# Kernel optimization log

Hardware: AMD Instinct MI355X
Metric: run time of the kernel (lower is better)

## Reference

```python
import jax, jax.numpy as jnp
import numpy as np

TAU_MEM = 20.0
TAU_SYN = 5.0
THRESHOLD = 1.0
SURROGATE_BETA = 4.0
RESET_POTENTIAL = 0.0

B, T, D_IN, H = 32, 1024, 512, 512


def setup_inputs() -> dict:
    key = jax.random.key(0)
    k1, k2 = jax.random.split(key)
    inputs = jax.random.normal(k1, (B, T, D_IN), dtype=jnp.float32)
    kernel = jax.random.normal(k2, (D_IN, H), dtype=jnp.float32) / np.sqrt(D_IN)
    bias = jnp.zeros((H,), dtype=jnp.float32)
    return {"inputs": inputs, "kernel": kernel, "bias": bias}


def reference(inputs, kernel, bias):
    batch = inputs.shape[0]
    hidden = kernel.shape[1]
    alpha_mem = jnp.exp(jnp.float32(-1.0 / TAU_MEM))
    alpha_syn = jnp.exp(jnp.float32(-1.0 / TAU_SYN))

    # Batch the per-step dense GEMM across time: [B,T,Din] @ [Din,H] -> [B,T,H]
    currents = jnp.einsum('bti,ih->bth', inputs, kernel) + bias
    currents_t = jnp.swapaxes(currents, 0, 1)  # [T,B,H] for scan

    def step(carry, ic):
        v_mem, i_syn = carry
        i_syn = alpha_syn * i_syn + ic
        v_mem = alpha_mem * v_mem + (1.0 - alpha_mem) * i_syn
        spikes = (v_mem >= THRESHOLD).astype(jnp.float32)
        surrogate = SURROGATE_BETA / (2.0 * (1.0 + jnp.cosh(SURROGATE_BETA * (v_mem - THRESHOLD))))
        spikes_with_grad = spikes + jax.lax.stop_gradient(spikes - surrogate)
        v_mem = jnp.where(spikes > 0, RESET_POTENTIAL, v_mem)
        return (v_mem, i_syn), (spikes_with_grad, v_mem)

    init = (jnp.zeros((batch, hidden), jnp.float32), jnp.zeros((batch, hidden), jnp.float32))
    (v_final, _), (spikes_t, vmem_t) = jax.lax.scan(step, init, currents_t)

    spike_output = jnp.swapaxes(spikes_t, 0, 1)      # [B,T,H]
    membrane_states = jnp.swapaxes(vmem_t, 0, 1)     # [B,T,H]
    spike_rate = jnp.mean(spike_output)
    return spike_output, membrane_states, v_final, spike_rate
```

## Files before the change

kernel.cpp:

```cpp
#include <hip/hip_runtime.h>

typedef unsigned short ushort_t;
typedef unsigned int   uint_t;
typedef float    float4v __attribute__((ext_vector_type(4)));
typedef _Float16 h16x8   __attribute__((ext_vector_type(8)));

#define Bsz 32
#define Tsz 1024
#define Din 512
#define Hsz 512
#define Mtot (Bsz * Tsz)
#define ELEMS ((size_t)Mtot * Hsz)

#define GLL16(gp, lp) __builtin_amdgcn_global_load_lds(                        \
    (const __attribute__((address_space(1))) unsigned int*)(gp),               \
    (__attribute__((address_space(3))) unsigned int*)(lp), 16, 0, 0)

#define GLL4(gp, lp) __builtin_amdgcn_global_load_lds(                         \
    (const __attribute__((address_space(1))) unsigned int*)(gp),               \
    (__attribute__((address_space(3))) unsigned int*)(lp), 4, 0, 0)

__global__ __launch_bounds__(256) void split_fp16x2(
    const float* __restrict__ A, const float* __restrict__ W,
    _Float16* __restrict__ Ah, _Float16* __restrict__ Bh)
{
    const int bid = blockIdx.x, tid = threadIdx.x;
    if (bid < 4096) {
        const size_t e   = ((size_t)bid * 256 + tid) * 16;
        const int    row = (int)(e >> 9);
        const int    col = (int)(e & 511);
        const float4* Af = (const float4*)(A + e);
        h16x8 v0a, v1a, v0b, v1b;
#pragma unroll
        for (int q = 0; q < 4; ++q) {
            float4 x = Af[q];
            const float c[4] = {x.x, x.y, x.z, x.w};
#pragma unroll
            for (int j = 0; j < 4; ++j) {
                const float xs = c[j] * 256.0f;
                const _Float16 h0 = (_Float16)xs;
                const float rf = xs - (float)h0;
                const _Float16 h1 = (_Float16)rf;
                const int idx = q * 4 + j;
                if (idx < 8) { v0a[idx] = h0; v1a[idx] = h1; }
                else         { v0b[idx - 8] = h0; v1b[idx - 8] = h1; }
            }
        }
        _Float16* d0 = Ah + (size_t)row * 1024 + col;
        *(h16x8*)(d0)           = v0a;
        *(h16x8*)(d0 + 8)       = v0b;
        *(h16x8*)(d0 + 512)     = v1a;
        *(h16x8*)(d0 + 512 + 8) = v1b;
    } else {
        const int f4 = (bid - 4096) * 256 + tid;
        const int k  = f4 >> 7;
        const int n4 = (f4 & 127) << 2;
        float4 x = *(const float4*)(W + (size_t)k * Hsz + n4);
        const float c[4] = {x.x, x.y, x.z, x.w};
#pragma unroll
        for (int j = 0; j < 4; ++j) {
            const float ws = c[j] * 2048.0f;
            const _Float16 h0 = (_Float16)ws;
            const float rf = ws - (float)h0;
            const _Float16 h1 = (_Float16)rf;
            _Float16* d = Bh + (size_t)(n4 + j) * 1024 + k;
            d[0]   = h0;
            d[512] = h1;
        }
    }
}

#define SA_STAGE(LIMB, KK, SLOTBASE) do {                                      \
    const char* g_ = Ag + (size_t)((LIMB) * 1024) + (size_t)((KK) * 64);       \
    _Pragma("unroll") for (int H = 0; H < 4; ++H)                              \
        GLL16(g_ + (size_t)H * 131072, ldsA + (SLOTBASE) + H * 4096 + lsd);    \
} while (0)

#define SB_STAGE(LIMB, KK, SLOT) do {                                          \
    const char* g_ = Bg + (size_t)((LIMB) * 1024) + (size_t)((KK) * 64);       \
    _Pragma("unroll") for (int H = 0; H < 2; ++H)                              \
        GLL16(g_ + (size_t)H * 131072, ldsB + (SLOT) * 8192 + H * 4096 + lsd); \
} while (0)

#define LD_AF(SLOTBASE) do {                                                   \
    _Pragma("unroll") for (int mf = 0; mf < 8; ++mf)                           \
        af[mf] = *(const h16x8*)(ldsA + (SLOTBASE) + (wm + mf * 16 + lr) * 64  \
                                 + physf * 16);                                \
} while (0)

#define LD_BF(DST, SLOT) do {                                                  \
    _Pragma("unroll") for (int nf = 0; nf < 4; ++nf)                           \
        DST[nf] = *(const h16x8*)(ldsB + (SLOT) * 8192 + (wn + nf * 16 + lr)   \
                                  * 64 + physf * 16);                          \
} while (0)

#define MFMAH(BF) do { __builtin_amdgcn_s_setprio(1);                          \
    _Pragma("unroll") for (int mf = 0; mf < 8; ++mf)                           \
    _Pragma("unroll") for (int nf = 0; nf < 4; ++nf)                           \
        acc[mf][nf] = __builtin_amdgcn_mfma_f32_16x16x32_f16(                  \
            af[mf], BF[nf], acc[mf][nf], 0, 0, 0);                             \
    __builtin_amdgcn_s_setprio(0); } while (0)

#define GATE(N) do { asm volatile("s_waitcnt vmcnt(" #N ")" ::: "memory");     \
    __builtin_amdgcn_sched_barrier(0); __builtin_amdgcn_s_barrier();           \
    asm volatile("" ::: "memory"); } while (0)

__global__ __launch_bounds__(256, 2) void gemm_f16k3(
    const _Float16* __restrict__ Ah, const _Float16* __restrict__ Bh,
    const float* __restrict__ bias, float* __restrict__ C)
{
    __shared__ __align__(16) char lds[65536];
    char* ldsA = lds;
    char* ldsB = lds + 32768;

    const int tid = threadIdx.x;
    const int bid = blockIdx.x;
    const int lin = ((bid & 7) << 6) | (bid >> 3);
    const int m0  = (lin >> 2) << 8;
    const int n0  = (lin & 3) << 7;
    const int w = tid >> 6, lane = tid & 63;
    const int wm = (w & 1) << 7;
    const int wn = (w >> 1) << 6;
    const int lr = lane & 15, lg = lane >> 4;

    const int physf = lg ^ (lr & 3) ^ ((lr >> 2) & 3);

    const int srow = tid >> 2;
    const int schk = tid & 3;
    const int logchk = schk ^ (srow & 3) ^ ((srow >> 2) & 3);
    const int lsd = tid * 16;
    const char* Ag = (const char*)Ah + (size_t)(m0 + srow) * 2048 + logchk * 16;
    const char* Bg = (const char*)Bh + (size_t)(n0 + srow) * 2048 + logchk * 16;

    float4v acc[8][4];
#pragma unroll
    for (int i = 0; i < 8; ++i)
#pragma unroll
        for (int j = 0; j < 4; ++j) acc[i][j] = (float4v)0.f;

    h16x8 af[8], bf0[4], bf1[4];

    SA_STAGE(0, 0, 0);
    SB_STAGE(0, 0, 0); SB_STAGE(1, 0, 1);
    SB_STAGE(0, 1, 2); SB_STAGE(1, 1, 3);
    GATE(0);

#pragma unroll 1
    for (int k = 0; k < 15; ++k) {
        const int s0 = (2 * k) & 3, s1 = (2 * k + 1) & 3;
        GATE(4);
        LD_AF(0); LD_BF(bf0, s0);
        SA_STAGE(1, k, 16384);
        MFMAH(bf0);
        GATE(4);
        LD_BF(bf1, s1);
        SA_STAGE(0, k + 1, 0);
        MFMAH(bf1);
        GATE(4);
        LD_AF(16384);
        if (k < 14) { SB_STAGE(0, k + 2, s0); SB_STAGE(1, k + 2, s1); }
        MFMAH(bf0);
    }
    {
        GATE(0);
        LD_AF(0); LD_BF(bf0, 2);
        SA_STAGE(1, 15, 16384);
        MFMAH(bf0);
        GATE(4);
        LD_BF(bf1, 3);
        MFMAH(bf1);
        GATE(0);
        LD_AF(16384);
        MFMAH(bf0);
    }

    constexpr float INVS = 1.0f / 524288.0f;
#pragma unroll
    for (int nf = 0; nf < 4; ++nf) {
        const int col = n0 + wn + nf * 16 + lr;
        const float bv = bias[col];
#pragma unroll
        for (int mf = 0; mf < 8; ++mf)
#pragma unroll
            for (int j = 0; j < 4; ++j) {
                const int row = m0 + wm + mf * 16 + lg * 4 + j;
                C[(size_t)row * Hsz + col] = fmaf(acc[mf][nf][j], INVS, bv);
            }
    }
}

#define BM 128
#define BN 128
#define BK 16
#define LDSA (BM + 4)
#define LDSB (BN + 4)
__global__ __launch_bounds__(256) void sgemm_currents(
    const float* __restrict__ A, const float* __restrict__ B,
    const float* __restrict__ bias, float* __restrict__ C)
{
    __shared__ float As[BK][LDSA];
    __shared__ float Bs[BK][LDSB];
    const int tid = threadIdx.x;
    const int tx = tid & 15, ty = tid >> 4;
    const int m0 = blockIdx.y * BM, n0 = blockIdx.x * BN;
    const int arow = tid >> 2, ac4 = (tid & 3) * 4;
    const int brow = tid >> 5, bc4 = (tid & 31) * 4;
    float acc[8][8];
#pragma unroll
    for (int i = 0; i < 8; ++i)
#pragma unroll
        for (int j = 0; j < 8; ++j) acc[i][j] = 0.f;
    const float* Abase = A + (size_t)(m0 + arow) * Din + ac4;
    const float* Bbase = B + (size_t)brow * Hsz + n0 + bc4;
    float4 a0 = *(const float4*)Abase;
    float4 a1 = *(const float4*)(Abase + (size_t)64 * Din);
    float4 b0 = *(const float4*)Bbase;
    float4 b1 = *(const float4*)(Bbase + (size_t)8 * Hsz);
    const int NKT = Din / BK;
    for (int kt = 0; kt < NKT; ++kt) {
        const float* apf = (const float*)&a0;
        const float* aqf = (const float*)&a1;
#pragma unroll
        for (int j = 0; j < 4; ++j) As[ac4 + j][arow] = apf[j];
#pragma unroll
        for (int j = 0; j < 4; ++j) As[ac4 + j][arow + 64] = aqf[j];
        *(float4*)&Bs[brow][bc4] = b0;
        *(float4*)&Bs[brow + 8][bc4] = b1;
        __syncthreads();
        if (kt + 1 < NKT) {
            const float* An = Abase + (kt + 1) * BK;
            const float* Bn = Bbase + (size_t)(kt + 1) * BK * Hsz;
            a0 = *(const float4*)An;
            a1 = *(const float4*)(An + (size_t)64 * Din);
            b0 = *(const float4*)Bn;
            b1 = *(const float4*)(Bn + (size_t)8 * Hsz);
        }
#pragma unroll
        for (int k = 0; k < BK; ++k) {
            float4 af0 = *(const float4*)&As[k][ty * 8];
            float4 af1 = *(const float4*)&As[k][ty * 8 + 4];
            float4 bf0 = *(const float4*)&Bs[k][tx * 8];
            float4 bf1 = *(const float4*)&Bs[k][tx * 8 + 4];
            const float av[8] = {af0.x, af0.y, af0.z, af0.w, af1.x, af1.y, af1.z, af1.w};
            const float bv[8] = {bf0.x, bf0.y, bf0.z, bf0.w, bf1.x, bf1.y, bf1.z, bf1.w};
#pragma unroll
            for (int i = 0; i < 8; ++i)
#pragma unroll
                for (int j = 0; j < 8; ++j) acc[i][j] = fmaf(av[i], bv[j], acc[i][j]);
        }
        __syncthreads();
    }
    const float4 bi0 = *(const float4*)&bias[n0 + tx * 8];
    const float4 bi1 = *(const float4*)&bias[n0 + tx * 8 + 4];
#pragma unroll
    for (int i = 0; i < 8; ++i) {
        const size_t row = (size_t)(m0 + ty * 8 + i);
        float4 o0 = make_float4(acc[i][0] + bi0.x, acc[i][1] + bi0.y,
                                acc[i][2] + bi0.z, acc[i][3] + bi0.w);
        float4 o1 = make_float4(acc[i][4] + bi1.x, acc[i][5] + bi1.y,
                                acc[i][6] + bi1.z, acc[i][7] + bi1.w);
        float* cp = C + row * Hsz + n0 + tx * 8;
        *(float4*)cp = o0;
        *(float4*)(cp + 4) = o1;
    }
}

__global__ __launch_bounds__(64) void lif_scan_g(
    const float* __restrict__ cur, float* __restrict__ spikes,
    float* __restrict__ vmem, float* __restrict__ vfinal,
    float* __restrict__ partials)
{
    __shared__ __align__(16) float lbuf[2][32][64];

    constexpr float A_M  = 0.95122942450071400910f;
    constexpr float OM_M = 1.0f - A_M;
    constexpr float A_S  = 0.81873075307798182354f;

    const int tid   = threadIdx.x;
    const int bid   = blockIdx.x;
    const int batch = bid >> 3;
    const int hbase = (bid & 7) << 6;
    const size_t sbase = (size_t)batch * (size_t)(Tsz * Hsz) + hbase + tid;

    const float* gsrc = cur + sbase;
    float* gspk = spikes + sbase;
    float* gvmm = vmem + sbase;

#pragma unroll
    for (int r = 0; r < 32; ++r)
        GLL4(gsrc + r * 512, &lbuf[0][r][0]);
    asm volatile("s_waitcnt vmcnt(0)" ::: "memory");
    __builtin_amdgcn_sched_barrier(0);

    float v = 0.f, isyn = 0.f, acc = 0.f;
    int pb = 0;
#pragma unroll 1
    for (int c = 0; c < 32; ++c) {
        if (c < 31) {
            const float* gs = gsrc + (size_t)(c + 1) * 16384;
            float (*db)[64] = lbuf[pb ^ 1];
#pragma unroll
            for (int r = 0; r < 32; ++r)
                GLL4(gs + r * 512, &db[r][0]);
        }
        const float* lrow = &lbuf[pb][0][tid];
        float* sp = gspk + (size_t)c * 16384;
        float* vp = gvmm + (size_t)c * 16384;
#pragma unroll
        for (int r = 0; r < 32; ++r) {
            isyn = fmaf(A_S, isyn, lrow[r * 64]);
            v    = fmaf(A_M, v, OM_M * isyn);
            const bool sb = (v >= 1.0f);
            float x = fminf(fmaf(4.0f, v, -4.0f), 30.0f);
            const float ep = __expf(x);
            const float tt = 1.0f + ep;
            const float rr = __builtin_amdgcn_rcpf(tt * tt);
            const float s2 = sb ? 2.0f : 0.0f;
            const float so = fmaf(-4.0f * ep, rr, s2);
            v = sb ? 0.0f : v;
            acc += so;
            sp[r * 512] = so;
            vp[r * 512] = v;
        }
        asm volatile("s_waitcnt vmcnt(63)" ::: "memory");
        __builtin_amdgcn_sched_barrier(0);
        pb ^= 1;
    }

    vfinal[bid * 64 + tid] = v;
#pragma unroll
    for (int o = 32; o; o >>= 1) acc += __shfl_down(acc, o);
    if (tid == 0) partials[blockIdx.x] = acc;
}

__device__ __forceinline__ void lif_step(float c, float& v, float& isyn,
                                         float& so_out)
{
    constexpr float A_M  = 0.95122942450071400910f;
    constexpr float OM_M = 1.0f - A_M;
    constexpr float A_S  = 0.81873075307798182354f;
    isyn = fmaf(A_S, isyn, c);
    v    = fmaf(A_M, v, OM_M * isyn);
    const float sp = (v >= 1.0f) ? 1.0f : 0.0f;
    float x = fmaf(4.0f, v, -4.0f);
    x = fminf(x, 30.0f);
    const float ep = __expf(x);
    const float tt = 1.0f + ep;
    const float surr = 4.0f * ep * __builtin_amdgcn_rcpf(tt * tt);
    so_out = fmaf(2.0f, sp, -surr);
    v = (sp > 0.f) ? 0.0f : v;
}

__global__ __launch_bounds__(64) void lif_scan(
    const float* cur, float* spikes, float* vmem, float* vfinal, float* partials)
{
    const int tid = threadIdx.x;
    const int gid = blockIdx.x * 64 + tid;
    const size_t base = ((size_t)(gid >> 9)) * (size_t)Tsz * Hsz + (gid & 511);

    float v = 0.f, isyn = 0.f, acc = 0.f;
    constexpr int P = 8;
    float ring[P];
#pragma unroll
    for (int p = 0; p < P; ++p) ring[p] = cur[base + (size_t)p * Hsz];

    for (int t = 0; t < Tsz; t += P) {
#pragma unroll
        for (int p = 0; p < P; ++p) {
            const float c = ring[p];
            int tn = t + P + p;
            tn = tn < (Tsz - 1) ? tn : (Tsz - 1);
            ring[p] = cur[base + (size_t)tn * Hsz];

            float so;
            lif_step(c, v, isyn, so);
            const size_t idx = base + (size_t)(t + p) * Hsz;
            spikes[idx] = so;
            vmem[idx]   = v;
            acc += so;
        }
    }
    vfinal[gid] = v;
#pragma unroll
    for (int off = 32; off; off >>= 1) acc += __shfl_down(acc, off);
    if (tid == 0) partials[blockIdx.x] = acc;
}

__global__ __launch_bounds__(256) void rate_finalize(
    const float* __restrict__ partials, float* __restrict__ rate)
{
    const int tid = threadIdx.x;
    float s = partials[tid];
#pragma unroll
    for (int off = 32; off; off >>= 1) s += __shfl_down(s, off);
    __shared__ float wsum[4];
    if ((tid & 63) == 0) wsum[tid >> 6] = s;
    __syncthreads();
    if (tid == 0)
        rate[0] = ((wsum[0] + wsum[1]) + (wsum[2] + wsum[3])) * (1.0f / 16777216.0f);
}

extern "C" void kernel_launch(void* const* d_in, const int* in_sizes, int n_in,
                              void* d_out, int out_size, void* d_ws, size_t ws_size,
                              hipStream_t stream)
{
    const float* inputs = (const float*)d_in[0];
    const float* weight = (const float*)d_in[1];
    const float* bias   = (const float*)d_in[2];

    float* out    = (float*)d_out;
    float* spikes = out;
    float* vmem   = out + ELEMS;
    float* vfinal = out + 2 * ELEMS;
    float* rate   = vfinal + (size_t)Bsz * Hsz;

    float* partials = (float*)d_ws;
    char*  ws       = (char*)d_ws;

    const size_t HDR   = 16384;
    const size_t CUR_B = ELEMS * 4;
    const size_t AH_B  = (size_t)Mtot * 1024 * 2;
    const size_t BH_B  = (size_t)Hsz * 1024 * 2;

    _Float16 *Ah, *Bh;
    float* cur;
    int path;
    if (ws_size >= HDR + CUR_B + AH_B + BH_B) {
        cur = (float*)(ws + HDR);
        Ah  = (_Float16*)(ws + HDR + CUR_B);
        Bh  = Ah + (size_t)Mtot * 1024;
        path = 0;
    } else if (ws_size >= HDR + CUR_B) {
        cur = (float*)(ws + HDR);
        Ah  = (_Float16*)d_out;
        Bh  = Ah + (size_t)Mtot * 1024;
        path = 1;
    } else {
        cur = vmem;
        Ah = Bh = nullptr;
        path = 2;
    }

    if (path != 2) {
        split_fp16x2<<<dim3(4096 + 256), 256, 0, stream>>>(inputs, weight, Ah, Bh);
        gemm_f16k3<<<dim3(512), 256, 0, stream>>>(Ah, Bh, bias, cur);
        lif_scan_g<<<dim3(256), 64, 0, stream>>>(cur, spikes, vmem, vfinal, partials);
    } else {
        sgemm_currents<<<dim3(4, 256), 256, 0, stream>>>(inputs, weight, bias, cur);
        lif_scan<<<dim3(256), 64, 0, stream>>>(cur, spikes, vmem, vfinal, partials);
    }
    rate_finalize<<<dim3(1), 256, 0, stream>>>(partials, rate);
}
```

Before: 150.0 us.

## Split LIF scan into producer and consumer wavefronts via LDS

The LIF scan kernel now runs two wavefronts per block. One loads currents and runs only the serial recurrence, writing pre-reset membrane values to a double-buffered LDS array. The other reads those values, computes spikes and surrogate outputs, and does the global stores and the rate reduction. The aim is to take the exp/rcp work and store traffic off the serial critical path so it overlaps with the recurrence. The cost is extra LDS, a block barrier per chunk, and a producer that waits on both vmcnt and lgkmcnt each chunk.

```diff
diff --git a/kernel.cpp b/kernel.cpp
--- a/kernel.cpp
+++ b/kernel.cpp
@@ -265,72 +265,95 @@
     }
 }
 
-__global__ __launch_bounds__(64) void lif_scan_g(
+__global__ __launch_bounds__(128) void lif_scan_pc(
     const float* __restrict__ cur, float* __restrict__ spikes,
     float* __restrict__ vmem, float* __restrict__ vfinal,
     float* __restrict__ partials)
 {
     __shared__ __align__(16) float lbuf[2][32][64];
+    __shared__ __align__(16) float pbuf[2][32][64];
 
     constexpr float A_M  = 0.95122942450071400910f;
     constexpr float OM_M = 1.0f - A_M;
     constexpr float A_S  = 0.81873075307798182354f;
 
-    const int tid   = threadIdx.x;
-    const int bid   = blockIdx.x;
+    const int tid  = threadIdx.x;
+    const int lane = tid & 63;
+    const int wv   = tid >> 6;
+    const int bid  = blockIdx.x;
     const int batch = bid >> 3;
     const int hbase = (bid & 7) << 6;
-    const size_t sbase = (size_t)batch * (size_t)(Tsz * Hsz) + hbase + tid;
-
-    const float* gsrc = cur + sbase;
-    float* gspk = spikes + sbase;
-    float* gvmm = vmem + sbase;
-
-#pragma unroll
-    for (int r = 0; r < 32; ++r)
-        GLL4(gsrc + r * 512, &lbuf[0][r][0]);
-    asm volatile("s_waitcnt vmcnt(0)" ::: "memory");
-    __builtin_amdgcn_sched_barrier(0);
-
-    float v = 0.f, isyn = 0.f, acc = 0.f;
-    int pb = 0;
+    const size_t sbase = (size_t)batch * (size_t)(Tsz * Hsz) + hbase + lane;
+
+    if (wv == 0) {
+        const float* gsrc = cur + sbase;
+#pragma unroll
+        for (int r = 0; r < 32; ++r)
+            GLL4(gsrc + r * 512, &lbuf[0][r][0]);
+        asm volatile("s_waitcnt vmcnt(0)" ::: "memory");
+        __builtin_amdgcn_sched_barrier(0);
+
+        float v = 0.f, isyn = 0.f;
 #pragma unroll 1
-    for (int c = 0; c < 32; ++c) {
-        if (c < 31) {
-            const float* gs = gsrc + (size_t)(c + 1) * 16384;
-            float (*db)[64] = lbuf[pb ^ 1];
-#pragma unroll
-            for (int r = 0; r < 32; ++r)
-                GLL4(gs + r * 512, &db[r][0]);
-        }
-        const float* lrow = &lbuf[pb][0][tid];
-        float* sp = gspk + (size_t)c * 16384;
-        float* vp = gvmm + (size_t)c * 16384;
-#pragma unroll
-        for (int r = 0; r < 32; ++r) {
-            isyn = fmaf(A_S, isyn, lrow[r * 64]);
-            v    = fmaf(A_M, v, OM_M * isyn);
-            const bool sb = (v >= 1.0f);
-            float x = fminf(fmaf(4.0f, v, -4.0f), 30.0f);
-            const float ep = __expf(x);
-            const float tt = 1.0f + ep;
-            const float rr = __builtin_amdgcn_rcpf(tt * tt);
-            const float s2 = sb ? 2.0f : 0.0f;
-            const float so = fmaf(-4.0f * ep, rr, s2);
-            v = sb ? 0.0f : v;
-            acc += so;
-            sp[r * 512] = so;
-            vp[r * 512] = v;
-        }
-        asm volatile("s_waitcnt vmcnt(63)" ::: "memory");
-        __builtin_amdgcn_sched_barrier(0);
-        pb ^= 1;
-    }
-
-    vfinal[bid * 64 + tid] = v;
-#pragma unroll
-    for (int o = 32; o; o >>= 1) acc += __shfl_down(acc, o);
-    if (tid == 0) partials[blockIdx.x] = acc;
+        for (int c = 0; c < 32; ++c) {
+            if (c < 31) {
+                const float* gs = gsrc + (size_t)(c + 1) * 16384;
+                float (*db)[64] = lbuf[(c + 1) & 1];
+#pragma unroll
+                for (int r = 0; r < 32; ++r)
+                    GLL4(gs + r * 512, &db[r][0]);
+            }
+            const float* lrow = &lbuf[c & 1][0][lane];
+            float* prow = &pbuf[c & 1][0][lane];
+#pragma unroll
+            for (int r = 0; r < 32; ++r) {
+                isyn = fmaf(A_S, isyn, lrow[r * 64]);
+                v    = fmaf(A_M, v, OM_M * isyn);
+                prow[r * 64] = v;
+                v = (v >= 1.0f) ? 0.0f : v;
+            }
+            asm volatile("s_waitcnt vmcnt(0) lgkmcnt(0)" ::: "memory");
+            __builtin_amdgcn_sched_barrier(0);
+            __builtin_amdgcn_s_barrier();
+            asm volatile("" ::: "memory");
+        }
+        vfinal[bid * 64 + lane] = v;
+        __builtin_amdgcn_s_barrier();
+    } else {
+        float* gspk = spikes + sbase;
+        float* gvmm = vmem + sbase;
+        float acc = 0.f;
+
+        __builtin_amdgcn_s_barrier();
+        asm volatile("" ::: "memory");
+#pragma unroll 1
+        for (int c = 0; c < 32; ++c) {
+            const float* prow = &pbuf[c & 1][0][lane];
+            float* sp = gspk + (size_t)c * 16384;
+            float* vp = gvmm + (size_t)c * 16384;
+#pragma unroll
+            for (int r = 0; r < 32; ++r) {
+                const float pv = prow[r * 64];
+                const bool sb = (pv >= 1.0f);
+                float x = fminf(fmaf(4.0f, pv, -4.0f), 30.0f);
+                const float ep = __expf(x);
+                const float tt = 1.0f + ep;
+                const float rr = __builtin_amdgcn_rcpf(tt * tt);
+                const float s2 = sb ? 2.0f : 0.0f;
+                const float so = fmaf(-4.0f * ep, rr, s2);
+                const float vo = sb ? 0.0f : pv;
+                acc += so;
+                sp[r * 512] = so;
+                vp[r * 512] = vo;
+            }
+            asm volatile("" ::: "memory");
+            __builtin_amdgcn_s_barrier();
+            asm volatile("" ::: "memory");
+        }
+#pragma unroll
+        for (int o = 32; o; o >>= 1) acc += __shfl_down(acc, o);
+        if (lane == 0) partials[bid] = acc;
+    }
 }
 
 __device__ __forceinline__ void lif_step(float c, float& v, float& isyn,
@@ -444,7 +467,7 @@
     if (path != 2) {
         split_fp16x2<<<dim3(4096 + 256), 256, 0, stream>>>(inputs, weight, Ah, Bh);
         gemm_f16k3<<<dim3(512), 256, 0, stream>>>(Ah, Bh, bias, cur);
-        lif_scan_g<<<dim3(256), 64, 0, stream>>>(cur, spikes, vmem, vfinal, partials);
+        lif_scan_pc<<<dim3(256), 128, 0, stream>>>(cur, spikes, vmem, vfinal, partials);
     } else {
         sgemm_currents<<<dim3(4, 256), 256, 0, stream>>>(inputs, weight, bias, cur);
         lif_scan<<<dim3(256), 64, 0, stream>>>(cur, spikes, vmem, vfinal, partials);
```

Result: faster. 139.2 us (-7.2%).
